# Optimization experiments

Hardware: AMD Instinct MI355X
Metric: run time of the kernel (lower is better)

## Reference

```python
import jax, jax.numpy as jnp
import numpy as np

N, E = 50000, 400000
IN, H, D, K = 256, 128, 64, 8
BN_EPS = 1e-5


def _gcn(x, row, col, W, b, n):
    # PyG GCNConv: x' = D^{-1/2} (A + I) D^{-1/2} (x @ W) + b
    h = x @ W
    loop = jnp.arange(n)
    r = jnp.concatenate([row, loop])
    c = jnp.concatenate([col, loop])
    deg = jax.ops.segment_sum(jnp.ones_like(c, dtype=h.dtype), c, num_segments=n)
    dinv = jnp.where(deg > 0, jax.lax.rsqrt(deg), 0.0)
    norm = dinv[r] * dinv[c]                      # [E+N]
    out = jax.ops.segment_sum(h[r] * norm[:, None], c, num_segments=n)
    return out + b


def setup_inputs() -> dict:
    key = jax.random.key(0)
    ks = jax.random.split(key, 10)
    x = jax.random.normal(ks[0], (N, IN), dtype=jnp.float32)
    edge_index = jax.random.randint(ks[1], (2, E), 0, N)
    s = 0.05
    return {
        "x": x,
        "edge_index": edge_index,
        "gamma": jnp.ones((IN,), jnp.float32),
        "beta": jnp.zeros((IN,), jnp.float32),
        "W1": jax.random.normal(ks[2], (IN, H), jnp.float32) * s,
        "b1": jnp.zeros((H,), jnp.float32),
        "W2": jax.random.normal(ks[3], (H, D), jnp.float32) * s,
        "b2": jnp.zeros((D,), jnp.float32),
        "Wt": jax.random.normal(ks[4], (D, D, K), jnp.float32) * s,
        "V": jax.random.normal(ks[5], (K, 2 * D), jnp.float32) * s,
        "bt": jax.random.normal(ks[6], (K, 1), jnp.float32) * s,
        "U": jax.random.normal(ks[7], (1, K), jnp.float32) * s,
    }


def reference(x, edge_index, gamma, beta, W1, b1, W2, b2, Wt, V, bt, U):
    row, col = edge_index[0], edge_index[1]
    # BatchNorm1d (training-mode batch stats, biased variance)
    mean = jnp.mean(x, axis=0)
    var = jnp.mean((x - mean) ** 2, axis=0)
    xn = (x - mean) * jax.lax.rsqrt(var + BN_EPS) * gamma + beta
    # encode: GCN -> leaky_relu(0.1) -> GCN
    h = _gcn(xn, row, col, W1, b1, N)
    h = jnp.where(h >= 0, h, 0.1 * h)
    z = _gcn(h, row, col, W2, b2, N)                 # [N, D]
    # decode: per-edge NTN bilinear + linear + tanh + U + sigmoid
    src = z[row]                                      # [E, D]
    dst = z[col]                                      # [E, D]
    bil = jnp.einsum('ed,dck,ec->ek', src, Wt, dst)   # [E, K] batched bilinear
    lin = jnp.concatenate([src, dst], axis=-1) @ V.T  # [E, K]
    t = jnp.tanh(bil + lin + bt[:, 0][None, :])       # [E, K] (dropout: eval mode)
    logits = t @ U[0]                                 # [E]
    return jax.nn.sigmoid(logits)
```

## Files before the change

### kernel.cpp

```cpp
#include <hip/hip_runtime.h>

#define NNODE 50000
#define NEDGE 400000

#define OFF_SUMS    0x0000
#define OFF_SUMSQ   0x0400
#define OFF_SCALE   0x0800
#define OFF_SHIFT   0x0C00
#define OFF_CSHIFT  0x1000
#define OFF_PART    0x1400
#define OFF_BPREF   0x1600
#define OFF_W1P     0x2000
#define OFF_WT2     0x22000
#define OFF_DEG     0x42000
#define OFF_OFFS    0x73000
#define OFF_CURS    0xA4000
#define OFF_DINV    0xD5000
#define OFF_CSR     0x106000
#define OFF_CSRE    0x290000
#define OFF_LV      0x420000
#define OFF_H0      0x800000
#define OFF_BNP     OFF_H0
#define OFF_Z0      OFF_H0
#define OFF_Z       (OFF_H0 + 0xD00000)
#define OFF_H1      0x2100000
#define OFF_Q       OFF_H1

#define BN_NB 1024
#define DEC_NB 2048

static __device__ __forceinline__ unsigned short f32_to_bf16(float f) {
  unsigned int u = __float_as_uint(f);
  u += 0x7fffu + ((u >> 16) & 1u);
  return (unsigned short)(u >> 16);
}

__global__ __launch_bounds__(256) void bn_stats1(const float* __restrict__ x,
                                                 float* __restrict__ P) {
  __shared__ float4 ls[4][64];
  __shared__ float4 lq[4][64];
  const int b = blockIdx.x, t = threadIdx.x;
  const int w = t >> 6, l = t & 63;
  const int rows = (NNODE + BN_NB - 1) / BN_NB;
  const int r0 = b * rows;
  const int r1 = min(NNODE, r0 + rows);
  float4 s = make_float4(0.f, 0.f, 0.f, 0.f);
  float4 q = make_float4(0.f, 0.f, 0.f, 0.f);
  for (int r = r0 + w; r < r1; r += 4) {
    float4 v = *(const float4*)(x + (size_t)r * 256 + l * 4);
    s.x += v.x; s.y += v.y; s.z += v.z; s.w += v.w;
    q.x = fmaf(v.x, v.x, q.x); q.y = fmaf(v.y, v.y, q.y);
    q.z = fmaf(v.z, v.z, q.z); q.w = fmaf(v.w, v.w, q.w);
  }
  ls[w][l] = s; lq[w][l] = q;
  __syncthreads();
  if (t < 64) {
    float4 s0 = ls[0][t], s1 = ls[1][t], s2 = ls[2][t], s3 = ls[3][t];
    float4 q0 = lq[0][t], q1 = lq[1][t], q2 = lq[2][t], q3 = lq[3][t];
    float4 ss = make_float4((s0.x + s1.x) + (s2.x + s3.x), (s0.y + s1.y) + (s2.y + s3.y),
                            (s0.z + s1.z) + (s2.z + s3.z), (s0.w + s1.w) + (s2.w + s3.w));
    float4 qq = make_float4((q0.x + q1.x) + (q2.x + q3.x), (q0.y + q1.y) + (q2.y + q3.y),
                            (q0.z + q1.z) + (q2.z + q3.z), (q0.w + q1.w) + (q2.w + q3.w));
    *(float4*)(P + (size_t)b * 512 + t * 4)       = ss;
    *(float4*)(P + (size_t)b * 512 + 256 + t * 4) = qq;
  }
}

__global__ __launch_bounds__(256) void bn_stats2(const float* __restrict__ P,
                                                 float* __restrict__ sums,
                                                 float* __restrict__ sumsq) {
  __shared__ float red[256];
  const int c = blockIdx.x, t = threadIdx.x;
  float s = 0.f;
  for (int i = t; i < BN_NB; i += 256) s += P[(size_t)i * 512 + c];
  red[t] = s;
  __syncthreads();
  if (t < 128) red[t] += red[t + 128];
  __syncthreads();
  if (t < 64) {
    float v = red[t] + red[t + 64];
    v += __shfl_down(v, 32);
    v += __shfl_down(v, 16);
    v += __shfl_down(v, 8);
    v += __shfl_down(v, 4);
    v += __shfl_down(v, 2);
    v += __shfl_down(v, 1);
    if (t == 0) {
      if (c < 256) sums[c] = v; else sumsq[c - 256] = v;
    }
  }
}

__global__ void bn_finalize(const float* __restrict__ sums, const float* __restrict__ sumsq,
                            const float* __restrict__ gamma, const float* __restrict__ beta,
                            float* __restrict__ scale, float* __restrict__ shift) {
  const int i = threadIdx.x;
  float mean = sums[i] * (1.f / NNODE);
  float var  = sumsq[i] * (1.f / NNODE) - mean * mean;
  float sc   = rsqrtf(var + 1e-5f) * gamma[i];
  scale[i] = sc;
  shift[i] = beta[i] - mean * sc;
}

__global__ void make_w1p(const float* __restrict__ W1, const float* __restrict__ scale,
                         float* __restrict__ W1p) {
  const int idx = blockIdx.x * 256 + threadIdx.x;
  W1p[idx] = scale[idx >> 7] * W1[idx];
}

__global__ void make_cshift(const float* __restrict__ W1, const float* __restrict__ shift,
                            float* __restrict__ cshift) {
  const int j = threadIdx.x;
  float s = 0.f;
  for (int i = 0; i < 256; ++i) s += shift[i] * W1[i * 128 + j];
  cshift[j] = s;
}

__global__ void make_wt2(const float* __restrict__ Wt, float* __restrict__ Wt2) {
  const int idx = blockIdx.x * 256 + threadIdx.x;
  const int d = idx >> 9, ck = idx & 511;
  const int c = ck >> 3, k = ck & 7;
  Wt2[c * 512 + d * 8 + k] = Wt[idx];
}

__global__ __launch_bounds__(256) void count_deg(const int* __restrict__ col, int* __restrict__ deg) {
  const int e = blockIdx.x * 256 + threadIdx.x;
  if (e < NEDGE) atomicAdd(&deg[col[e]], 1);
}

__global__ __launch_bounds__(1024) void scan_a(const int* __restrict__ deg, int* __restrict__ offs,
                                               int* __restrict__ partials, float* __restrict__ dinv) {
  __shared__ int buf[1024];
  const int t = threadIdx.x;
  const int i = blockIdx.x * 1024 + t;
  const int v = (i < NNODE) ? deg[i] : 0;
  buf[t] = v;
  __syncthreads();
  for (int off = 1; off < 1024; off <<= 1) {
    int a = (t >= off) ? buf[t - off] : 0;
    __syncthreads();
    buf[t] += a;
    __syncthreads();
  }
  if (i < NNODE) {
    offs[i] = buf[t] - v;
    dinv[i] = rsqrtf((float)(v + 1));
  }
  if (t == 1023) partials[blockIdx.x] = buf[t];
}

__global__ void scan_b(const int* __restrict__ partials, int* __restrict__ bpref,
                       int* __restrict__ offs) {
  if (threadIdx.x == 0) {
    int run = 0;
    for (int b = 0; b < 49; ++b) { bpref[b] = run; run += partials[b]; }
    offs[NNODE] = run;
  }
}

__global__ __launch_bounds__(1024) void scan_c(int* __restrict__ offs, const int* __restrict__ bpref,
                                               int* __restrict__ cursor) {
  const int i = blockIdx.x * 1024 + threadIdx.x;
  if (i < NNODE) {
    int o = offs[i] + bpref[blockIdx.x];
    offs[i] = o;
    cursor[i] = o;
  }
}

__global__ __launch_bounds__(256) void fill_csr(const int* __restrict__ row, const int* __restrict__ col,
                                                int* __restrict__ cursor, int* __restrict__ csr_src,
                                                int* __restrict__ csr_eid) {
  const int e = blockIdx.x * 256 + threadIdx.x;
  if (e < NEDGE) {
    int c = col[e];
    int p = atomicAdd(&cursor[c], 1);
    csr_src[p] = row[e];
    csr_eid[p] = e;
  }
}

template <int BM, int BN, int BK, int TM, int TN, bool BF16OUT>
__global__ __launch_bounds__(256) void gemm_tiled(const float* __restrict__ A,
                                                  const float* __restrict__ B,
                                                  void* __restrict__ Cout,
                                                  const float* __restrict__ bias,
                                                  const float* __restrict__ rowscale,
                                                  int M, int Kd, int Nd) {
  constexpr int TX = BN / TN;
  constexpr int TY = BM / TM;
  constexpr int THREADS = TX * TY;
  __shared__ __align__(16) float As[BM][BK + 4];
  __shared__ __align__(16) float Bs[BK][BN];
  const int tid = threadIdx.x;
  const int tx = tid % TX, ty = tid / TX;
  const int m0 = blockIdx.x * BM, n0 = blockIdx.y * BN;

  float acc[TM][TN];
  for (int i = 0; i < TM; ++i)
    for (int j = 0; j < TN; ++j) acc[i][j] = 0.f;

  for (int k0 = 0; k0 < Kd; k0 += BK) {
    for (int i = tid; i < (BM * BK) / 4; i += THREADS) {
      int mm = i / (BK / 4), kq = i % (BK / 4);
      int gm = m0 + mm;
      float4 v = make_float4(0.f, 0.f, 0.f, 0.f);
      if (gm < M) v = *(const float4*)(A + (size_t)gm * Kd + k0 + kq * 4);
      *(float4*)(&As[mm][kq * 4]) = v;
    }
    for (int i = tid; i < (BK * BN) / 4; i += THREADS) {
      int kk = i / (BN / 4), nq = i % (BN / 4);
      *(float4*)(&Bs[kk][nq * 4]) = *(const float4*)(B + (size_t)(k0 + kk) * Nd + n0 + nq * 4);
    }
    __syncthreads();
#pragma unroll
    for (int kk = 0; kk < BK; ++kk) {
      float a[TM], b[TN];
#pragma unroll
      for (int i = 0; i < TM; ++i) a[i] = As[ty * TM + i][kk];
#pragma unroll
      for (int j4 = 0; j4 < TN / 4; ++j4) {
        float4 bv = *(const float4*)(&Bs[kk][tx * TN + j4 * 4]);
        b[j4 * 4 + 0] = bv.x; b[j4 * 4 + 1] = bv.y; b[j4 * 4 + 2] = bv.z; b[j4 * 4 + 3] = bv.w;
      }
#pragma unroll
      for (int i = 0; i < TM; ++i)
#pragma unroll
        for (int j = 0; j < TN; ++j) acc[i][j] = fmaf(a[i], b[j], acc[i][j]);
    }
    __syncthreads();
  }

  float bv[TN];
#pragma unroll
  for (int j = 0; j < TN; ++j) bv[j] = bias ? bias[n0 + tx * TN + j] : 0.f;

#pragma unroll
  for (int i = 0; i < TM; ++i) {
    int gm = m0 + ty * TM + i;
    if (gm >= M) continue;
    const float rs = rowscale ? rowscale[gm] : 1.f;
    if constexpr (BF16OUT) {
      unsigned short* C = (unsigned short*)Cout;
      alignas(16) unsigned short tmp[TN];
#pragma unroll
      for (int j = 0; j < TN; ++j) tmp[j] = f32_to_bf16((acc[i][j] + bv[j]) * rs);
      if constexpr (TN == 8) {
        *(uint4*)(C + (size_t)gm * Nd + n0 + tx * TN) = *(const uint4*)tmp;
      } else {
#pragma unroll
        for (int j = 0; j < TN; ++j) C[(size_t)gm * Nd + n0 + tx * TN + j] = tmp[j];
      }
    } else {
      float* C = (float*)Cout;
#pragma unroll
      for (int j4 = 0; j4 < TN / 4; ++j4) {
        float4 v;
        v.x = (acc[i][j4 * 4 + 0] + bv[j4 * 4 + 0]) * rs;
        v.y = (acc[i][j4 * 4 + 1] + bv[j4 * 4 + 1]) * rs;
        v.z = (acc[i][j4 * 4 + 2] + bv[j4 * 4 + 2]) * rs;
        v.w = (acc[i][j4 * 4 + 3] + bv[j4 * 4 + 3]) * rs;
        *(float4*)(C + (size_t)gm * Nd + n0 + tx * TN + j4 * 4) = v;
      }
    }
  }
}

template <int F, bool LEAKY>
__global__ __launch_bounds__(256) void agg_kernel(const float* __restrict__ hs,
                                                  const int* __restrict__ csr_src,
                                                  const int* __restrict__ offs,
                                                  const float* __restrict__ dinv,
                                                  const float* __restrict__ bias,
                                                  float* __restrict__ out) {
  constexpr int NPB = 256 / F;
  const int vth = blockIdx.x * NPB + threadIdx.x / F;
  const int v = __builtin_amdgcn_readfirstlane(vth);
  const int f = threadIdx.x % F;
  const float dv = dinv[v];
  const int j0 = offs[v], j1 = offs[v + 1];

  float a0 = hs[(size_t)v * F + f];
  float a1 = 0.f, a2 = 0.f, a3 = 0.f;

  for (int jb = j0; jb < j1; jb += 4) {
    const int jm = j1 - 1;
    const int r0 = csr_src[jb];
    const int r1 = csr_src[min(jb + 1, jm)];
    const int r2 = csr_src[min(jb + 2, jm)];
    const int r3 = csr_src[min(jb + 3, jm)];
    const float w1 = (jb + 1 <= jm) ? 1.f : 0.f;
    const float w2 = (jb + 2 <= jm) ? 1.f : 0.f;
    const float w3 = (jb + 3 <= jm) ? 1.f : 0.f;
    a0 += hs[(size_t)r0 * F + f];
    a1 = fmaf(w1, hs[(size_t)r1 * F + f], a1);
    a2 = fmaf(w2, hs[(size_t)r2 * F + f], a2);
    a3 = fmaf(w3, hs[(size_t)r3 * F + f], a3);
  }

  float o = ((a0 + a1) + (a2 + a3)) * dv + bias[f];
  if (LEAKY) o = (o >= 0.f) ? o : 0.1f * o;
  out[(size_t)v * F + f] = o;
}

__global__ __launch_bounds__(256) void lv_kernel(const float* __restrict__ z,
                                                 const float* __restrict__ V,
                                                 float* __restrict__ LV) {
  const int idx = blockIdx.x * 256 + threadIdx.x;
  if (idx >= NNODE * 16) return;
  const int v = idx >> 4, kk = idx & 15;
  const float* vr = V + (kk & 7) * 128 + ((kk & 8) ? 64 : 0);
  const float* zr = z + (size_t)v * 64;
  float s = 0.f;
#pragma unroll
  for (int d4 = 0; d4 < 16; ++d4) {
    float4 zv = *(const float4*)(zr + d4 * 4);
    float4 vv = *(const float4*)(vr + d4 * 4);
    s += zv.x * vv.x + zv.y * vv.y + zv.z * vv.z + zv.w * vv.w;
  }
  LV[idx] = s;
}

__global__ __launch_bounds__(256) void decode_kernel(const int* __restrict__ csr_src,
                                                     const int* __restrict__ csr_eid,
                                                     const int* __restrict__ offs,
                                                     const float* __restrict__ z,
                                                     const unsigned short* __restrict__ Q,
                                                     const float* __restrict__ LV,
                                                     const float* __restrict__ bt,
                                                     const float* __restrict__ U,
                                                     float* __restrict__ out) {
  __shared__ float qs[4][512];
  const int w = threadIdx.x >> 6, lane = threadIdx.x & 63;
  const int g = lane >> 3, k = lane & 7;
  const float uk = U[k];
  const float btk = bt[k];
  constexpr int NWAVES = DEC_NB * 4;

  for (int v = blockIdx.x * 4 + w; v < NNODE; v += NWAVES) {
    {
      union { uint4 r; unsigned short u[8]; } uu;
      uu.r = *(const uint4*)(Q + (size_t)v * 512 + lane * 8);
      float4 lo, hi;
      lo.x = __uint_as_float(((unsigned int)uu.u[0]) << 16);
      lo.y = __uint_as_float(((unsigned int)uu.u[1]) << 16);
      lo.z = __uint_as_float(((unsigned int)uu.u[2]) << 16);
      lo.w = __uint_as_float(((unsigned int)uu.u[3]) << 16);
      hi.x = __uint_as_float(((unsigned int)uu.u[4]) << 16);
      hi.y = __uint_as_float(((unsigned int)uu.u[5]) << 16);
      hi.z = __uint_as_float(((unsigned int)uu.u[6]) << 16);
      hi.w = __uint_as_float(((unsigned int)uu.u[7]) << 16);
      *(float4*)(&qs[w][lane * 8])     = lo;
      *(float4*)(&qs[w][lane * 8 + 4]) = hi;
    }

    const float lvc = LV[(size_t)v * 16 + 8 + k] + btk;
    const int j0 = offs[v], j1 = offs[v + 1];

    for (int jb = j0; jb < j1; jb += 8) {
      const int j = jb + g;
      const bool act = (j < j1);
      const int r = act ? csr_src[j] : 0;
      const int eid = act ? csr_eid[j] : 0;
      const float4* zr = (const float4*)(z + (size_t)r * 64);
      float acc = 0.f;
#pragma unroll
      for (int d4 = 0; d4 < 16; ++d4) {
        float4 zv = zr[d4];
        const float* qp = &qs[w][d4 * 32 + k];
        acc = fmaf(zv.x, qp[0], acc);
        acc = fmaf(zv.y, qp[8], acc);
        acc = fmaf(zv.z, qp[16], acc);
        acc = fmaf(zv.w, qp[24], acc);
      }
      acc += LV[(size_t)r * 16 + k] + lvc;
      float c = tanhf(acc) * uk;
      c += __shfl_xor(c, 1);
      c += __shfl_xor(c, 2);
      c += __shfl_xor(c, 4);
      if (act && k == 0) out[eid] = 1.f / (1.f + __expf(-c));
    }
  }
}

extern "C" void kernel_launch(void* const* d_in, const int* in_sizes, int n_in,
                              void* d_out, int out_size, void* d_ws, size_t ws_size,
                              hipStream_t stream) {
  const float* x     = (const float*)d_in[0];
  const int*   ei    = (const int*)d_in[1];
  const float* gamma = (const float*)d_in[2];
  const float* beta  = (const float*)d_in[3];
  const float* W1    = (const float*)d_in[4];
  const float* b1    = (const float*)d_in[5];
  const float* W2    = (const float*)d_in[6];
  const float* b2    = (const float*)d_in[7];
  const float* Wt    = (const float*)d_in[8];
  const float* V     = (const float*)d_in[9];
  const float* bt    = (const float*)d_in[10];
  const float* U     = (const float*)d_in[11];
  float* out = (float*)d_out;
  char* ws = (char*)d_ws;

  const int* row = ei;
  const int* col = ei + NEDGE;

  float* sums   = (float*)(ws + OFF_SUMS);
  float* sumsq  = (float*)(ws + OFF_SUMSQ);
  float* scale  = (float*)(ws + OFF_SCALE);
  float* shiftv = (float*)(ws + OFF_SHIFT);
  float* cshift = (float*)(ws + OFF_CSHIFT);
  int*   part   = (int*)(ws + OFF_PART);
  int*   bpref  = (int*)(ws + OFF_BPREF);
  float* W1p    = (float*)(ws + OFF_W1P);
  float* Wt2    = (float*)(ws + OFF_WT2);
  int*   deg    = (int*)(ws + OFF_DEG);
  int*   offs   = (int*)(ws + OFF_OFFS);
  int*   curs   = (int*)(ws + OFF_CURS);
  float* dinv   = (float*)(ws + OFF_DINV);
  int*   csr    = (int*)(ws + OFF_CSR);
  int*   csre   = (int*)(ws + OFF_CSRE);
  float* LV     = (float*)(ws + OFF_LV);
  float* bnp    = (float*)(ws + OFF_BNP);
  float* h0     = (float*)(ws + OFF_H0);
  float* h1     = (float*)(ws + OFF_H1);
  float* z0     = (float*)(ws + OFF_Z0);
  float* zz     = (float*)(ws + OFF_Z);
  unsigned short* Q = (unsigned short*)(ws + OFF_Q);

  hipMemsetAsync(ws + OFF_DEG, 0, NNODE * 4, stream);

  bn_stats1<<<BN_NB, 256, 0, stream>>>(x, bnp);
  count_deg<<<1563, 256, 0, stream>>>(col, deg);
  bn_stats2<<<512, 256, 0, stream>>>(bnp, sums, sumsq);
  bn_finalize<<<1, 256, 0, stream>>>(sums, sumsq, gamma, beta, scale, shiftv);
  make_w1p<<<128, 256, 0, stream>>>(W1, scale, W1p);
  make_cshift<<<1, 128, 0, stream>>>(W1, shiftv, cshift);
  make_wt2<<<128, 256, 0, stream>>>(Wt, Wt2);

  scan_a<<<49, 1024, 0, stream>>>(deg, offs, part, dinv);
  scan_b<<<1, 64, 0, stream>>>(part, bpref, offs);
  scan_c<<<49, 1024, 0, stream>>>(offs, bpref, curs);
  fill_csr<<<1563, 256, 0, stream>>>(row, col, curs, csr, csre);

  gemm_tiled<64, 128, 32, 4, 8, false><<<dim3(782, 1), 256, 0, stream>>>(x, W1p, h0, cshift, dinv, NNODE, 256, 128);
  agg_kernel<128, true><<<25000, 256, 0, stream>>>(h0, csr, offs, dinv, b1, h1);
  gemm_tiled<64, 64, 32, 4, 4, false><<<dim3(782, 1), 256, 0, stream>>>(h1, W2, z0, nullptr, dinv, NNODE, 128, 64);
  agg_kernel<64, false><<<12500, 256, 0, stream>>>(z0, csr, offs, dinv, b2, zz);

  gemm_tiled<64, 128, 32, 4, 8, true><<<dim3(782, 4), 256, 0, stream>>>(zz, Wt2, Q, nullptr, nullptr, NNODE, 64, 512);
  lv_kernel<<<3125, 256, 0, stream>>>(zz, V, LV);

  decode_kernel<<<DEC_NB, 256, 0, stream>>>(csr, csre, offs, zz, Q, LV, bt, U, out);
}
```

Measured before the change: 465.8 us.

## Hold per-node Q slice in registers with k-major layout in decode

Changes the Wt reorder so each node's Q row is laid out k-major with contiguous d. Each decode lane now loads its own 64 bf16 Q values straight into registers, removing the shared-memory staging and the per-edge LDS reads. The dot product is split across four accumulators to shorten the FMA dependency chain. Workspace offsets for Q and Z are moved to fit the layout. The 64-float register array raises VGPR pressure and may lower occupancy, and the Q loads are now duplicated across the 8 edge groups in a wave.

```diff
diff --git a/kernel.cpp b/kernel.cpp
--- a/kernel.cpp
+++ b/kernel.cpp
@@ -22,9 +22,9 @@
 #define OFF_H0      0x800000
 #define OFF_BNP     OFF_H0
 #define OFF_Z0      OFF_H0
-#define OFF_Z       (OFF_H0 + 0xD00000)
 #define OFF_H1      0x2100000
-#define OFF_Q       OFF_H1
+#define OFF_Z       0x3A00000
+#define OFF_Q       OFF_H0
 
 #define BN_NB 1024
 #define DEC_NB 2048
@@ -116,11 +116,11 @@
   cshift[j] = s;
 }
 
-__global__ void make_wt2(const float* __restrict__ Wt, float* __restrict__ Wt2) {
+__global__ void make_wt2(const float* __restrict__ Wt, float* __restrict__ Wt3) {
   const int idx = blockIdx.x * 256 + threadIdx.x;
   const int d = idx >> 9, ck = idx & 511;
   const int c = ck >> 3, k = ck & 7;
-  Wt2[c * 512 + d * 8 + k] = Wt[idx];
+  Wt3[c * 512 + k * 64 + d] = Wt[idx];
 }
 
 __global__ __launch_bounds__(256) void count_deg(const int* __restrict__ col, int* __restrict__ deg) {
@@ -325,12 +325,11 @@
                                                      const int* __restrict__ csr_eid,
                                                      const int* __restrict__ offs,
                                                      const float* __restrict__ z,
-                                                     const unsigned short* __restrict__ Q,
+                                                     const unsigned short* __restrict__ Qt,
                                                      const float* __restrict__ LV,
                                                      const float* __restrict__ bt,
                                                      const float* __restrict__ U,
                                                      float* __restrict__ out) {
-  __shared__ float qs[4][512];
   const int w = threadIdx.x >> 6, lane = threadIdx.x & 63;
   const int g = lane >> 3, k = lane & 7;
   const float uk = U[k];
@@ -338,20 +337,15 @@
   constexpr int NWAVES = DEC_NB * 4;
 
   for (int v = blockIdx.x * 4 + w; v < NNODE; v += NWAVES) {
-    {
-      union { uint4 r; unsigned short u[8]; } uu;
-      uu.r = *(const uint4*)(Q + (size_t)v * 512 + lane * 8);
-      float4 lo, hi;
-      lo.x = __uint_as_float(((unsigned int)uu.u[0]) << 16);
-      lo.y = __uint_as_float(((unsigned int)uu.u[1]) << 16);
-      lo.z = __uint_as_float(((unsigned int)uu.u[2]) << 16);
-      lo.w = __uint_as_float(((unsigned int)uu.u[3]) << 16);
-      hi.x = __uint_as_float(((unsigned int)uu.u[4]) << 16);
-      hi.y = __uint_as_float(((unsigned int)uu.u[5]) << 16);
-      hi.z = __uint_as_float(((unsigned int)uu.u[6]) << 16);
-      hi.w = __uint_as_float(((unsigned int)uu.u[7]) << 16);
-      *(float4*)(&qs[w][lane * 8])     = lo;
-      *(float4*)(&qs[w][lane * 8 + 4]) = hi;
+    float qv[64];
+    const uint2* qp = (const uint2*)(Qt + (size_t)v * 512 + k * 64);
+#pragma unroll
+    for (int d4 = 0; d4 < 16; ++d4) {
+      uint2 qq = qp[d4];
+      qv[d4 * 4 + 0] = __uint_as_float(qq.x << 16);
+      qv[d4 * 4 + 1] = __uint_as_float(qq.x & 0xFFFF0000u);
+      qv[d4 * 4 + 2] = __uint_as_float(qq.y << 16);
+      qv[d4 * 4 + 3] = __uint_as_float(qq.y & 0xFFFF0000u);
     }
 
     const float lvc = LV[(size_t)v * 16 + 8 + k] + btk;
@@ -363,17 +357,16 @@
       const int r = act ? csr_src[j] : 0;
       const int eid = act ? csr_eid[j] : 0;
       const float4* zr = (const float4*)(z + (size_t)r * 64);
-      float acc = 0.f;
+      float a0 = 0.f, a1 = 0.f, a2 = 0.f, a3 = 0.f;
 #pragma unroll
       for (int d4 = 0; d4 < 16; ++d4) {
         float4 zv = zr[d4];
-        const float* qp = &qs[w][d4 * 32 + k];
-        acc = fmaf(zv.x, qp[0], acc);
-        acc = fmaf(zv.y, qp[8], acc);
-        acc = fmaf(zv.z, qp[16], acc);
-        acc = fmaf(zv.w, qp[24], acc);
+        a0 = fmaf(zv.x, qv[d4 * 4 + 0], a0);
+        a1 = fmaf(zv.y, qv[d4 * 4 + 1], a1);
+        a2 = fmaf(zv.z, qv[d4 * 4 + 2], a2);
+        a3 = fmaf(zv.w, qv[d4 * 4 + 3], a3);
       }
-      acc += LV[(size_t)r * 16 + k] + lvc;
+      float acc = ((a0 + a1) + (a2 + a3)) + LV[(size_t)r * 16 + k] + lvc;
       float c = tanhf(acc) * uk;
       c += __shfl_xor(c, 1);
       c += __shfl_xor(c, 2);
@@ -412,7 +405,7 @@
   int*   part   = (int*)(ws + OFF_PART);
   int*   bpref  = (int*)(ws + OFF_BPREF);
   float* W1p    = (float*)(ws + OFF_W1P);
-  float* Wt2    = (float*)(ws + OFF_WT2);
+  float* Wt3    = (float*)(ws + OFF_WT2);
   int*   deg    = (int*)(ws + OFF_DEG);
   int*   offs   = (int*)(ws + OFF_OFFS);
   int*   curs   = (int*)(ws + OFF_CURS);
@@ -435,7 +428,7 @@
   bn_finalize<<<1, 256, 0, stream>>>(sums, sumsq, gamma, beta, scale, shiftv);
   make_w1p<<<128, 256, 0, stream>>>(W1, scale, W1p);
   make_cshift<<<1, 128, 0, stream>>>(W1, shiftv, cshift);
-  make_wt2<<<128, 256, 0, stream>>>(Wt, Wt2);
+  make_wt2<<<128, 256, 0, stream>>>(Wt, Wt3);
 
   scan_a<<<49, 1024, 0, stream>>>(deg, offs, part, dinv);
   scan_b<<<1, 64, 0, stream>>>(part, bpref, offs);
@@ -447,7 +440,7 @@
   gemm_tiled<64, 64, 32, 4, 4, false><<<dim3(782, 1), 256, 0, stream>>>(h1, W2, z0, nullptr, dinv, NNODE, 128, 64);
   agg_kernel<64, false><<<12500, 256, 0, stream>>>(z0, csr, offs, dinv, b2, zz);
 
-  gemm_tiled<64, 128, 32, 4, 8, true><<<dim3(782, 4), 256, 0, stream>>>(zz, Wt2, Q, nullptr, nullptr, NNODE, 64, 512);
+  gemm_tiled<64, 128, 32, 4, 8, true><<<dim3(782, 4), 256, 0, stream>>>(zz, Wt3, Q, nullptr, nullptr, NNODE, 64, 512);
   lv_kernel<<<3125, 256, 0, stream>>>(zz, V, LV);
 
   decode_kernel<<<DEC_NB, 256, 0, stream>>>(csr, csre, offs, zz, Q, LV, bt, U, out);
```

Measured after the change: 495.5 us. 6.4% more time.
